# Kernel optimization log

Hardware: AMD Instinct MI355X
Metric: run time of the kernel (lower is better)

## Reference

```python
import jax, jax.numpy as jnp
import numpy as np
import math

D_MODEL = 512
NHEAD = 8
D_K = D_MODEL // NHEAD
WINDOW = 128
BATCH = 1
SEQ = 4096
NEG = -1e9  # matches torch masked_fill value


def setup_inputs() -> dict:
    key = jax.random.key(0)
    ks = jax.random.split(key, 9)
    s = 1.0 / math.sqrt(D_MODEL)
    return {
        "x": jax.random.normal(ks[0], (BATCH, SEQ, D_MODEL), dtype=jnp.float32),
        "wq": jax.random.uniform(ks[1], (D_MODEL, D_MODEL), jnp.float32, -s, s),
        "bq": jax.random.uniform(ks[2], (D_MODEL,), jnp.float32, -s, s),
        "wk": jax.random.uniform(ks[3], (D_MODEL, D_MODEL), jnp.float32, -s, s),
        "bk": jax.random.uniform(ks[4], (D_MODEL,), jnp.float32, -s, s),
        "wv": jax.random.uniform(ks[5], (D_MODEL, D_MODEL), jnp.float32, -s, s),
        "bv": jax.random.uniform(ks[6], (D_MODEL,), jnp.float32, -s, s),
        "wo": jax.random.uniform(ks[7], (D_MODEL, D_MODEL), jnp.float32, -s, s),
        "bo": jax.random.uniform(ks[8], (D_MODEL,), jnp.float32, -s, s),
    }


def reference(x, wq, bq, wk, bk, wv, bv, wo, bo):
    B, S, D = x.shape
    # projections -> (B, H, S, d_k)
    q = (x @ wq.T + bq).reshape(B, S, NHEAD, D_K).transpose(0, 2, 1, 3)
    k = (x @ wk.T + bk).reshape(B, S, NHEAD, D_K).transpose(0, 2, 1, 3)
    v = (x @ wv.T + bv).reshape(B, S, NHEAD, D_K).transpose(0, 2, 1, 3)
    # dense scores, band-masked (faithful to original: full S x S)
    scores = jnp.einsum('bhqd,bhkd->bhqk', q, k) / math.sqrt(D_K)
    idx = jnp.arange(S)
    band = jnp.abs(idx[:, None] - idx[None, :]) <= WINDOW  # (S, S)
    scores = jnp.where(band[None, None], scores, NEG)
    attn = jax.nn.softmax(scores, axis=-1)  # (B, H, S, S)
    ctx = jnp.einsum('bhqk,bhkd->bhqd', attn, v)
    ctx = ctx.transpose(0, 2, 1, 3).reshape(B, S, D)
    out = ctx @ wo.T + bo
    return out, attn
```

## Files before the change

kernel.cpp:

```cpp
#include <hip/hip_runtime.h>
#include <hip/hip_bf16.h>
#include <math.h>

#define S 4096
#define D 512
#define H 8
#define DK 64
#define WIN 128

typedef __attribute__((ext_vector_type(8))) short bf16x8;
typedef __attribute__((ext_vector_type(4))) float f32x4;

__device__ __forceinline__ unsigned short f2bf(float f) {
    __hip_bfloat16 h = __float2bfloat16(f);
    return *(unsigned short*)&h;
}

__global__ __launch_bounds__(256) void conv_bf16_kernel(
    const float* __restrict__ in, unsigned short* __restrict__ out, int n)
{
    const int i = (blockIdx.x * 256 + threadIdx.x) * 8;
    if (i >= n) return;
    float4 a = *(const float4*)&in[i];
    float4 b = *(const float4*)&in[i + 4];
    ushort4 o0 = {f2bf(a.x), f2bf(a.y), f2bf(a.z), f2bf(a.w)};
    ushort4 o1 = {f2bf(b.x), f2bf(b.y), f2bf(b.z), f2bf(b.w)};
    *(ushort4*)&out[i]     = o0;
    *(ushort4*)&out[i + 4] = o1;
}

__device__ __forceinline__ void mfma_gemm_body(
    const unsigned short* __restrict__ A,
    const float* __restrict__ W,
    const float* __restrict__ bias,
    float* __restrict__ C,
    unsigned short* __restrict__ CB)
{
    __shared__ unsigned short Bs[64][520];

    const int tid  = threadIdx.x;
    const int m0   = blockIdx.x * 128;
    const int n0   = blockIdx.y * 64;
    const int wv   = tid >> 6;
    const int lane = tid & 63;
    const int l16  = lane & 15;
    const int klo  = (lane >> 4) * 8;

    #pragma unroll
    for (int it = 0; it < 16; ++it) {
        const int c   = tid + it * 256;
        const int row = c >> 6;
        const int kc  = (c & 63) * 8;
        const float* src = &W[(size_t)(n0 + row) * 512 + kc];
        float4 a = *(const float4*)&src[0];
        float4 b = *(const float4*)&src[4];
        ushort4 o0 = {f2bf(a.x), f2bf(a.y), f2bf(a.z), f2bf(a.w)};
        ushort4 o1 = {f2bf(b.x), f2bf(b.y), f2bf(b.z), f2bf(b.w)};
        *(ushort4*)&Bs[row][kc]     = o0;
        *(ushort4*)&Bs[row][kc + 4] = o1;
    }
    __syncthreads();

    const unsigned short* arow0 = &A[(size_t)(m0 + wv * 32 + l16) * 512 + klo];
    const unsigned short* arow1 = arow0 + 16 * 512;

    f32x4 acc[2][4];
    #pragma unroll
    for (int r = 0; r < 2; ++r)
        #pragma unroll
        for (int nf = 0; nf < 4; ++nf)
            acc[r][nf] = (f32x4){0.f, 0.f, 0.f, 0.f};

    #pragma unroll 4
    for (int kb = 0; kb < 512; kb += 32) {
        bf16x8 a0 = *(const bf16x8*)&arow0[kb];
        bf16x8 a1 = *(const bf16x8*)&arow1[kb];
        #pragma unroll
        for (int nf = 0; nf < 4; ++nf) {
            bf16x8 b = *(const bf16x8*)&Bs[nf * 16 + l16][kb + klo];
            acc[0][nf] = __builtin_amdgcn_mfma_f32_16x16x32_bf16(a0, b, acc[0][nf], 0, 0, 0);
            acc[1][nf] = __builtin_amdgcn_mfma_f32_16x16x32_bf16(a1, b, acc[1][nf], 0, 0, 0);
        }
    }

    const int r0 = (lane >> 4) * 4;
    #pragma unroll
    for (int r = 0; r < 2; ++r) {
        #pragma unroll
        for (int nf = 0; nf < 4; ++nf) {
            const int col = n0 + nf * 16 + l16;
            const float bb = bias[col];
            #pragma unroll
            for (int vv = 0; vv < 4; ++vv) {
                const int row = m0 + wv * 32 + r * 16 + r0 + vv;
                const float val = acc[r][nf][vv] + bb;
                if (C)  C [(size_t)row * 512 + col] = val;
                if (CB) CB[(size_t)row * 512 + col] = f2bf(val);
            }
        }
    }
}

__global__ __launch_bounds__(256) void proj3_kernel(
    const unsigned short* __restrict__ xb,
    const float* __restrict__ wq, const float* __restrict__ bq,
    const float* __restrict__ wk, const float* __restrict__ bk,
    const float* __restrict__ wv, const float* __restrict__ bv,
    unsigned short* __restrict__ qb, unsigned short* __restrict__ kb,
    unsigned short* __restrict__ vb)
{
    const float* W; const float* b; unsigned short* CB;
    if (blockIdx.z == 0)      { W = wq; b = bq; CB = qb; }
    else if (blockIdx.z == 1) { W = wk; b = bk; CB = kb; }
    else                      { W = wv; b = bv; CB = vb; }
    mfma_gemm_body(xb, W, b, nullptr, CB);
}

__global__ __launch_bounds__(256) void outproj_kernel(
    const unsigned short* __restrict__ ctxb,
    const float* __restrict__ wo, const float* __restrict__ bo,
    float* __restrict__ out)
{
    mfma_gemm_body(ctxb, wo, bo, out, nullptr);
}

__global__ __launch_bounds__(256) void band_attn_kernel(
    const unsigned short* __restrict__ qb, const unsigned short* __restrict__ kb,
    float* __restrict__ attn)
{
    __shared__ __align__(16) unsigned short Qs[16][72];
    __shared__ __align__(16) unsigned short Kb[64][72];
    __shared__ float P[16][336];
    __shared__ float rinvs[16];

    const int tid = threadIdx.x;
    const int h  = blockIdx.y;
    const int q0 = blockIdx.x * 16;
    const int w0 = q0 - 128;

    const int wv   = tid >> 6;
    const int lane = tid & 63;
    const int l16  = lane & 15;
    const int klo  = (lane >> 4) * 8;
    const int r0   = (lane >> 4) * 4;

    {
        const int row = tid >> 4;
        const int db  = (tid & 15) * 4;
        *(ushort4*)&Qs[row][db] =
            *(const ushort4*)&qb[(size_t)(q0 + row) * 512 + h * 64 + db];
    }

    const int lr = tid >> 2;
    const int ld = (tid & 3) * 16;

    for (int ch = 0; ch < 5; ++ch) {
        const int c0 = w0 + ch * 64;
        if (c0 + 64 <= 0 || c0 >= S) continue;
        __syncthreads();
        {
            const int krow = min(max(c0 + lr, 0), S - 1);
            const unsigned short* src = &kb[(size_t)krow * 512 + h * 64 + ld];
            *(bf16x8*)&Kb[lr][ld]     = *(const bf16x8*)&src[0];
            *(bf16x8*)&Kb[lr][ld + 8] = *(const bf16x8*)&src[8];
        }
        __syncthreads();

        f32x4 acc = (f32x4){0.f, 0.f, 0.f, 0.f};
        #pragma unroll
        for (int kk = 0; kk < 64; kk += 32) {
            bf16x8 a = *(const bf16x8*)&Qs[l16][kk + klo];
            bf16x8 b = *(const bf16x8*)&Kb[wv * 16 + l16][kk + klo];
            acc = __builtin_amdgcn_mfma_f32_16x16x32_bf16(a, b, acc, 0, 0, 0);
        }
        #pragma unroll
        for (int vv = 0; vv < 4; ++vv)
            P[r0 + vv][ch * 64 + wv * 16 + l16] = acc[vv] * 0.125f;
    }
    __syncthreads();

    {
        const int r   = tid >> 4;
        const int lx  = tid & 15;
        const int i   = q0 + r;
        const int lo = max(i - WIN, 0) - w0;
        const int hi = min(i + WIN, S - 1) - w0;

        float m = -1e30f;
        for (int c = lo + lx; c <= hi; c += 16) m = fmaxf(m, P[r][c]);
        m = fmaxf(m, __shfl_xor(m, 1));
        m = fmaxf(m, __shfl_xor(m, 2));
        m = fmaxf(m, __shfl_xor(m, 4));
        m = fmaxf(m, __shfl_xor(m, 8));

        float sum = 0.f;
        for (int c = lo + lx; c <= hi; c += 16) {
            float e = __expf(P[r][c] - m);
            P[r][c] = e;
            sum += e;
        }
        sum += __shfl_xor(sum, 1);
        sum += __shfl_xor(sum, 2);
        sum += __shfl_xor(sum, 4);
        sum += __shfl_xor(sum, 8);
        if (lx == 0) rinvs[r] = 1.0f / sum;
    }
    __syncthreads();

    float* rowbase = attn + (size_t)h * S * S;
    #pragma unroll 1
    for (int r = 0; r < 16; ++r) {
        const int i = q0 + r;
        float* rowp = rowbase + (size_t)i * S;
        const int lo = max(i - WIN, 0) - w0;
        const int hi = min(i + WIN, S - 1) - w0;
        const float rv = rinvs[r];
        #pragma unroll
        for (int t = 0; t < 4; ++t) {
            const int c4 = (tid + t * 256) << 2;
            const int lc = c4 - w0;
            float4 o;
            if (lc >= lo && lc + 3 <= hi) {
                float4 p = *(const float4*)&P[r][lc];
                o.x = p.x * rv; o.y = p.y * rv; o.z = p.z * rv; o.w = p.w * rv;
            } else if (lc + 3 < lo || lc > hi) {
                o = make_float4(0.f, 0.f, 0.f, 0.f);
            } else {
                o.x = (lc + 0 >= lo && lc + 0 <= hi) ? P[r][lc + 0] * rv : 0.f;
                o.y = (lc + 1 >= lo && lc + 1 <= hi) ? P[r][lc + 1] * rv : 0.f;
                o.z = (lc + 2 >= lo && lc + 2 <= hi) ? P[r][lc + 2] * rv : 0.f;
                o.w = (lc + 3 >= lo && lc + 3 <= hi) ? P[r][lc + 3] * rv : 0.f;
            }
            *(float4*)&rowp[c4] = o;
        }
    }
}

__global__ __launch_bounds__(256) void band_pv_kernel(
    const float* __restrict__ attn, const unsigned short* __restrict__ vb,
    unsigned short* __restrict__ ctxb)
{
    __shared__ unsigned short Pb [64][328];
    __shared__ unsigned short VsT[64][328];
    const int tid = threadIdx.x;
    const int h  = blockIdx.y;
    const int q0 = blockIdx.x * 64;
    const int w0 = q0 - 128;

    const int lr = tid >> 2;
    const int ld = (tid & 3) * 16;
    const float* aptr = attn + (size_t)h * S * S;

    for (int ch = 0; ch < 5; ++ch) {
        const int c0 = w0 + ch * 64;
        if (c0 >= 0 && c0 < S) {
            #pragma unroll
            for (int t = 0; t < 4; ++t) {
                float4 p4 = *(const float4*)&aptr[(size_t)(q0 + lr) * S + c0 + ld + t * 4];
                ushort4 o = {f2bf(p4.x), f2bf(p4.y), f2bf(p4.z), f2bf(p4.w)};
                *(ushort4*)&Pb[lr][ch * 64 + ld + t * 4] = o;
                ushort4 v4 = *(const ushort4*)&vb[(size_t)(c0 + lr) * 512 + h * 64 + ld + t * 4];
                VsT[ld + t * 4 + 0][ch * 64 + lr] = v4.x;
                VsT[ld + t * 4 + 1][ch * 64 + lr] = v4.y;
                VsT[ld + t * 4 + 2][ch * 64 + lr] = v4.z;
                VsT[ld + t * 4 + 3][ch * 64 + lr] = v4.w;
            }
        } else {
            #pragma unroll
            for (int t = 0; t < 4; ++t) {
                ushort4 z4 = {0, 0, 0, 0};
                *(ushort4*)&Pb[lr][ch * 64 + ld + t * 4] = z4;
                VsT[ld + t * 4 + 0][ch * 64 + lr] = 0;
                VsT[ld + t * 4 + 1][ch * 64 + lr] = 0;
                VsT[ld + t * 4 + 2][ch * 64 + lr] = 0;
                VsT[ld + t * 4 + 3][ch * 64 + lr] = 0;
            }
        }
    }
    __syncthreads();

    const int wv   = tid >> 6;
    const int lane = tid & 63;
    const int l16  = lane & 15;
    const int klo  = (lane >> 4) * 8;

    f32x4 acc[4];
    #pragma unroll
    for (int nf = 0; nf < 4; ++nf) acc[nf] = (f32x4){0.f, 0.f, 0.f, 0.f};

    #pragma unroll
    for (int ks = 0; ks < 10; ++ks) {
        bf16x8 a = *(const bf16x8*)&Pb[wv * 16 + l16][ks * 32 + klo];
        #pragma unroll
        for (int nf = 0; nf < 4; ++nf) {
            bf16x8 b = *(const bf16x8*)&VsT[nf * 16 + l16][ks * 32 + klo];
            acc[nf] = __builtin_amdgcn_mfma_f32_16x16x32_bf16(a, b, acc[nf], 0, 0, 0);
        }
    }

    const int r0 = (lane >> 4) * 4;
    #pragma unroll
    for (int nf = 0; nf < 4; ++nf) {
        #pragma unroll
        for (int vv = 0; vv < 4; ++vv) {
            const int row = q0 + wv * 16 + r0 + vv;
            ctxb[(size_t)row * 512 + h * 64 + nf * 16 + l16] = f2bf(acc[nf][vv]);
        }
    }
}

extern "C" void kernel_launch(void* const* d_in, const int* in_sizes, int n_in,
                              void* d_out, int out_size, void* d_ws, size_t ws_size,
                              hipStream_t stream)
{
    (void)in_sizes; (void)n_in; (void)out_size; (void)ws_size;
    const float* x  = (const float*)d_in[0];
    const float* wq = (const float*)d_in[1];
    const float* bq = (const float*)d_in[2];
    const float* wk = (const float*)d_in[3];
    const float* bk = (const float*)d_in[4];
    const float* wv = (const float*)d_in[5];
    const float* bv = (const float*)d_in[6];
    const float* wo = (const float*)d_in[7];
    const float* bo = (const float*)d_in[8];

    float* out  = (float*)d_out;
    float* attn = out + (size_t)S * D;

    unsigned short* xb   = (unsigned short*)d_ws;
    unsigned short* qb   = xb   + (size_t)S * D;
    unsigned short* kb   = qb   + (size_t)S * D;
    unsigned short* vb   = kb   + (size_t)S * D;
    unsigned short* ctxb = vb   + (size_t)S * D;

    conv_bf16_kernel<<<(S * D) / (256 * 8), 256, 0, stream>>>(x, xb, S * D);
    proj3_kernel<<<dim3(32, 8, 3), 256, 0, stream>>>(xb, wq, bq, wk, bk, wv, bv, qb, kb, vb);
    band_attn_kernel<<<dim3(256, 8), 256, 0, stream>>>(qb, kb, attn);
    band_pv_kernel<<<dim3(64, 8), 256, 0, stream>>>(attn, vb, ctxb);
    outproj_kernel<<<dim3(32, 8), 256, 0, stream>>>(ctxb, wo, bo, out);
}
```

Before: 159.3 us.

## Fuse P·V into band attention kernel, dropping separate PV kernel

Computes the P·V product inside the band attention kernel from the unnormalized exponentials held in shared memory, then scales by the row reciprocal and writes ctx directly. This removes the separate PV kernel, which re-read the band of the attention matrix from global memory, along with one launch. In exchange, V is loaded and transposed per 16-query block instead of per 64-query block, adding redundant V traffic and scalar LDS transposes. The softmax loop now zeros out-of-band entries.

```diff
diff --git a/kernel.cpp b/kernel.cpp
--- a/kernel.cpp
+++ b/kernel.cpp
@@ -126,10 +126,11 @@
 
 __global__ __launch_bounds__(256) void band_attn_kernel(
     const unsigned short* __restrict__ qb, const unsigned short* __restrict__ kb,
-    float* __restrict__ attn)
+    const unsigned short* __restrict__ vb,
+    float* __restrict__ attn, unsigned short* __restrict__ ctxb)
 {
     __shared__ __align__(16) unsigned short Qs[16][72];
-    __shared__ __align__(16) unsigned short Kb[64][72];
+    __shared__ __align__(16) unsigned short KV[64][72];
     __shared__ float P[16][336];
     __shared__ float rinvs[16];
 
@@ -161,8 +162,8 @@
         {
             const int krow = min(max(c0 + lr, 0), S - 1);
             const unsigned short* src = &kb[(size_t)krow * 512 + h * 64 + ld];
-            *(bf16x8*)&Kb[lr][ld]     = *(const bf16x8*)&src[0];
-            *(bf16x8*)&Kb[lr][ld + 8] = *(const bf16x8*)&src[8];
+            *(bf16x8*)&KV[lr][ld]     = *(const bf16x8*)&src[0];
+            *(bf16x8*)&KV[lr][ld + 8] = *(const bf16x8*)&src[8];
         }
         __syncthreads();
 
@@ -170,7 +171,7 @@
         #pragma unroll
         for (int kk = 0; kk < 64; kk += 32) {
             bf16x8 a = *(const bf16x8*)&Qs[l16][kk + klo];
-            bf16x8 b = *(const bf16x8*)&Kb[wv * 16 + l16][kk + klo];
+            bf16x8 b = *(const bf16x8*)&KV[wv * 16 + l16][kk + klo];
             acc = __builtin_amdgcn_mfma_f32_16x16x32_bf16(a, b, acc, 0, 0, 0);
         }
         #pragma unroll
@@ -194,10 +195,13 @@
         m = fmaxf(m, __shfl_xor(m, 8));
 
         float sum = 0.f;
-        for (int c = lo + lx; c <= hi; c += 16) {
-            float e = __expf(P[r][c] - m);
+        for (int c = lx; c < 320; c += 16) {
+            float e = 0.f;
+            if (c >= lo && c <= hi) {
+                e = __expf(P[r][c] - m);
+                sum += e;
+            }
             P[r][c] = e;
-            sum += e;
         }
         sum += __shfl_xor(sum, 1);
         sum += __shfl_xor(sum, 2);
@@ -205,7 +209,47 @@
         sum += __shfl_xor(sum, 8);
         if (lx == 0) rinvs[r] = 1.0f / sum;
     }
-    __syncthreads();
+
+    f32x4 pacc = (f32x4){0.f, 0.f, 0.f, 0.f};
+    for (int ch = 0; ch < 5; ++ch) {
+        const int c0 = w0 + ch * 64;
+        if (c0 + 64 <= 0 || c0 >= S) continue;
+        __syncthreads();
+        {
+            const int vrow = min(max(c0 + lr, 0), S - 1);
+            ushort4 v0 = *(const ushort4*)&vb[(size_t)vrow * 512 + h * 64 + ld];
+            ushort4 v1 = *(const ushort4*)&vb[(size_t)vrow * 512 + h * 64 + ld + 4];
+            ushort4 v2 = *(const ushort4*)&vb[(size_t)vrow * 512 + h * 64 + ld + 8];
+            ushort4 v3 = *(const ushort4*)&vb[(size_t)vrow * 512 + h * 64 + ld + 12];
+            KV[ld +  0][lr] = v0.x; KV[ld +  1][lr] = v0.y;
+            KV[ld +  2][lr] = v0.z; KV[ld +  3][lr] = v0.w;
+            KV[ld +  4][lr] = v1.x; KV[ld +  5][lr] = v1.y;
+            KV[ld +  6][lr] = v1.z; KV[ld +  7][lr] = v1.w;
+            KV[ld +  8][lr] = v2.x; KV[ld +  9][lr] = v2.y;
+            KV[ld + 10][lr] = v2.z; KV[ld + 11][lr] = v2.w;
+            KV[ld + 12][lr] = v3.x; KV[ld + 13][lr] = v3.y;
+            KV[ld + 14][lr] = v3.z; KV[ld + 15][lr] = v3.w;
+        }
+        __syncthreads();
+
+        #pragma unroll
+        for (int kk = 0; kk < 64; kk += 32) {
+            unsigned short abuf[8];
+            #pragma unroll
+            for (int e = 0; e < 8; ++e)
+                abuf[e] = f2bf(P[l16][ch * 64 + kk + klo + e]);
+            bf16x8 a = *(const bf16x8*)abuf;
+            bf16x8 b = *(const bf16x8*)&KV[wv * 16 + l16][kk + klo];
+            pacc = __builtin_amdgcn_mfma_f32_16x16x32_bf16(a, b, pacc, 0, 0, 0);
+        }
+    }
+
+    #pragma unroll
+    for (int vv = 0; vv < 4; ++vv) {
+        const int row = q0 + r0 + vv;
+        ctxb[(size_t)row * 512 + h * 64 + wv * 16 + l16] =
+            f2bf(pacc[vv] * rinvs[r0 + vv]);
+    }
 
     float* rowbase = attn + (size_t)h * S * S;
     #pragma unroll 1
@@ -236,79 +280,6 @@
     }
 }
 
-__global__ __launch_bounds__(256) void band_pv_kernel(
-    const float* __restrict__ attn, const unsigned short* __restrict__ vb,
-    unsigned short* __restrict__ ctxb)
-{
-    __shared__ unsigned short Pb [64][328];
-    __shared__ unsigned short VsT[64][328];
-    const int tid = threadIdx.x;
-    const int h  = blockIdx.y;
-    const int q0 = blockIdx.x * 64;
-    const int w0 = q0 - 128;
-
-    const int lr = tid >> 2;
-    const int ld = (tid & 3) * 16;
-    const float* aptr = attn + (size_t)h * S * S;
-
-    for (int ch = 0; ch < 5; ++ch) {
-        const int c0 = w0 + ch * 64;
-        if (c0 >= 0 && c0 < S) {
-            #pragma unroll
-            for (int t = 0; t < 4; ++t) {
-                float4 p4 = *(const float4*)&aptr[(size_t)(q0 + lr) * S + c0 + ld + t * 4];
-                ushort4 o = {f2bf(p4.x), f2bf(p4.y), f2bf(p4.z), f2bf(p4.w)};
-                *(ushort4*)&Pb[lr][ch * 64 + ld + t * 4] = o;
-                ushort4 v4 = *(const ushort4*)&vb[(size_t)(c0 + lr) * 512 + h * 64 + ld + t * 4];
-                VsT[ld + t * 4 + 0][ch * 64 + lr] = v4.x;
-                VsT[ld + t * 4 + 1][ch * 64 + lr] = v4.y;
-                VsT[ld + t * 4 + 2][ch * 64 + lr] = v4.z;
-                VsT[ld + t * 4 + 3][ch * 64 + lr] = v4.w;
-            }
-        } else {
-            #pragma unroll
-            for (int t = 0; t < 4; ++t) {
-                ushort4 z4 = {0, 0, 0, 0};
-                *(ushort4*)&Pb[lr][ch * 64 + ld + t * 4] = z4;
-                VsT[ld + t * 4 + 0][ch * 64 + lr] = 0;
-                VsT[ld + t * 4 + 1][ch * 64 + lr] = 0;
-                VsT[ld + t * 4 + 2][ch * 64 + lr] = 0;
-                VsT[ld + t * 4 + 3][ch * 64 + lr] = 0;
-            }
-        }
-    }
-    __syncthreads();
-
-    const int wv   = tid >> 6;
-    const int lane = tid & 63;
-    const int l16  = lane & 15;
-    const int klo  = (lane >> 4) * 8;
-
-    f32x4 acc[4];
-    #pragma unroll
-    for (int nf = 0; nf < 4; ++nf) acc[nf] = (f32x4){0.f, 0.f, 0.f, 0.f};
-
-    #pragma unroll
-    for (int ks = 0; ks < 10; ++ks) {
-        bf16x8 a = *(const bf16x8*)&Pb[wv * 16 + l16][ks * 32 + klo];
-        #pragma unroll
-        for (int nf = 0; nf < 4; ++nf) {
-            bf16x8 b = *(const bf16x8*)&VsT[nf * 16 + l16][ks * 32 + klo];
-            acc[nf] = __builtin_amdgcn_mfma_f32_16x16x32_bf16(a, b, acc[nf], 0, 0, 0);
-        }
-    }
-
-    const int r0 = (lane >> 4) * 4;
-    #pragma unroll
-    for (int nf = 0; nf < 4; ++nf) {
-        #pragma unroll
-        for (int vv = 0; vv < 4; ++vv) {
-            const int row = q0 + wv * 16 + r0 + vv;
-            ctxb[(size_t)row * 512 + h * 64 + nf * 16 + l16] = f2bf(acc[nf][vv]);
-        }
-    }
-}
-
 extern "C" void kernel_launch(void* const* d_in, const int* in_sizes, int n_in,
                               void* d_out, int out_size, void* d_ws, size_t ws_size,
                               hipStream_t stream)
@@ -335,7 +306,6 @@
 
     conv_bf16_kernel<<<(S * D) / (256 * 8), 256, 0, stream>>>(x, xb, S * D);
     proj3_kernel<<<dim3(32, 8, 3), 256, 0, stream>>>(xb, wq, bq, wk, bk, wv, bv, qb, kb, vb);
-    band_attn_kernel<<<dim3(256, 8), 256, 0, stream>>>(qb, kb, attn);
-    band_pv_kernel<<<dim3(64, 8), 256, 0, stream>>>(attn, vb, ctxb);
+    band_attn_kernel<<<dim3(256, 8), 256, 0, stream>>>(qb, kb, vb, attn, ctxb);
     outproj_kernel<<<dim3(32, 8), 256, 0, stream>>>(ctxb, wo, bo, out);
 }
```

Measured after the change: 153.3 us. 3.8% less time.
